# Kernel optimization log

Hardware: AMD Instinct MI355X
Metric: run time of the kernel (lower is better)

## Reference

```python
import jax, jax.numpy as jnp
import numpy as np

N_NODES = 50000
N_EDGES = 800000
IN_C, HID_C, OUT_C = 128, 128, 40


def gcn_conv(x, W, b, src, dst, dinv):
    # x: [N, Fin] -> [N, Fout]; PyG GCNConv: h = W x, then sym-normalized
    # aggregation over edges (incl. self-loops), plus bias.
    h = x @ W  # [N, Fout]
    norm = dinv[src] * dinv[dst]  # [E+N]
    msg = h[src] * norm[:, None]  # gather + scale, [E+N, Fout]
    out = jax.ops.segment_sum(msg, dst, num_segments=x.shape[0])
    return out + b


def _prep_edges(edge_index, n):
    # add self-loops; compute deg^{-1/2} with unit edge weights
    loop = jnp.arange(n, dtype=edge_index.dtype)
    src = jnp.concatenate([edge_index[0], loop])
    dst = jnp.concatenate([edge_index[1], loop])
    deg = jax.ops.segment_sum(jnp.ones_like(dst, dtype=jnp.float32), dst, num_segments=n)
    dinv = jnp.where(deg > 0, jax.lax.rsqrt(jnp.maximum(deg, 1.0)), 0.0)
    return src, dst, dinv


def setup_inputs() -> dict:
    key = jax.random.key(0)
    ks = jax.random.split(key, 5)
    x = jax.random.normal(ks[0], (N_NODES, IN_C), dtype=jnp.float32)
    edge_index = jax.random.randint(ks[1], (2, N_EDGES), 0, N_NODES, dtype=jnp.int32)
    s = 0.05
    W1 = jax.random.normal(ks[2], (IN_C, HID_C), dtype=jnp.float32) * s
    W2 = jax.random.normal(ks[3], (HID_C, HID_C), dtype=jnp.float32) * s
    W3 = jax.random.normal(ks[4], (HID_C, OUT_C), dtype=jnp.float32) * s
    return {
        "x": x, "edge_index": edge_index,
        "W1": W1, "b1": jnp.zeros((HID_C,), jnp.float32),
        "W2": W2, "b2": jnp.zeros((HID_C,), jnp.float32),
        "W3": W3, "b3": jnp.zeros((OUT_C,), jnp.float32),
    }


def reference(x, edge_index, W1, b1, W2, b2, W3, b3):
    n = x.shape[0]
    src, dst, dinv = _prep_edges(edge_index, n)
    h = jax.nn.relu(gcn_conv(x, W1, b1, src, dst, dinv))  # dropout = id (eval)
    h = jax.nn.relu(gcn_conv(h, W2, b2, src, dst, dinv))
    h = gcn_conv(h, W3, b3, src, dst, dinv)
    return jax.nn.log_softmax(h, axis=1)
```

## Files before the change

### kernel.cpp

```cpp
#include <hip/hip_runtime.h>
#include <cmath>

__device__ __forceinline__ unsigned short f2bf(float f) {
  unsigned u = __float_as_uint(f);
  u = (u + 0x7FFFu + ((u >> 16) & 1u)) >> 16;
  return (unsigned short)u;
}
__device__ __forceinline__ unsigned pack2(float a, float b) {
  return (unsigned)f2bf(a) | ((unsigned)f2bf(b) << 16);
}
__device__ __forceinline__ float bflo(unsigned u) { return __uint_as_float(u << 16); }
__device__ __forceinline__ float bfhi(unsigned u) { return __uint_as_float(u & 0xFFFF0000u); }
__device__ __forceinline__ float bf1(unsigned short h) { return __uint_as_float((unsigned)h << 16); }

using bh8 = __attribute__((ext_vector_type(8))) short;
using f32x4 = __attribute__((ext_vector_type(4))) float;

#define BK_STRIDE 8192

__global__ __launch_bounds__(256) void k_f2b(const float* __restrict__ x, unsigned short* __restrict__ xb, int total4) {
  int i = blockIdx.x * 256 + threadIdx.x;
  if (i < total4) {
    float4 v = *(const float4*)&x[(size_t)i * 4];
    uint2 o;
    o.x = pack2(v.x, v.y);
    o.y = pack2(v.z, v.w);
    *(uint2*)&xb[(size_t)i * 4] = o;
  }
}

__global__ __launch_bounds__(256) void k_bin(const int* __restrict__ src, const int* __restrict__ dst,
                                             int* __restrict__ bucketCur, unsigned* __restrict__ bucketBuf,
                                             int E, int chunk) {
  __shared__ int hist[256], base[256], cur[256];
  int t = threadIdx.x;
  hist[t] = 0;
  cur[t] = 0;
  __syncthreads();
  int s0 = blockIdx.x * chunk;
  int s1 = min(E, s0 + chunk);
  for (int i = s0 + t; i < s1; i += 256) atomicAdd(&hist[dst[i] >> 8], 1);
  __syncthreads();
  if (hist[t] > 0) base[t] = atomicAdd(&bucketCur[t], hist[t]);
  __syncthreads();
  for (int i = s0 + t; i < s1; i += 256) {
    int d = dst[i];
    int b = d >> 8;
    int r = base[b] + atomicAdd(&cur[b], 1);
    if (r < BK_STRIDE)
      bucketBuf[(size_t)b * BK_STRIDE + r] = (unsigned)src[i] | ((unsigned)(d & 255) << 16);
  }
}

__global__ __launch_bounds__(256) void k_bucket_scan(const int* __restrict__ bucketCur, int* __restrict__ bucketBase,
                                                     int* __restrict__ rp, int nbk, int n, int E) {
  __shared__ int s[256];
  int t = threadIdx.x;
  int v = (t < nbk) ? bucketCur[t] : 0;
  s[t] = v;
  __syncthreads();
  for (int off = 1; off < 256; off <<= 1) {
    int u = (t >= off) ? s[t - off] : 0;
    __syncthreads();
    s[t] += u;
    __syncthreads();
  }
  if (t < nbk) bucketBase[t] = s[t] - v;
  if (t == 0) rp[n] = E;
}

__global__ __launch_bounds__(256) void k_build(const unsigned* __restrict__ bucketBuf,
                                               const int* __restrict__ bucketCnt,
                                               const int* __restrict__ bucketBase, int* __restrict__ rp,
                                               float* __restrict__ dinv, int* __restrict__ csr, int n) {
  __shared__ int hist[256], excl[256], cur[256], s[256];
  int b = blockIdx.x, t = threadIdx.x;
  int cntE = bucketCnt[b];
  int e0 = bucketBase[b];
  const unsigned* buf = bucketBuf + (size_t)b * BK_STRIDE;
  hist[t] = 0;
  cur[t] = 0;
  __syncthreads();
  for (int i = t; i < cntE; i += 256) atomicAdd(&hist[(buf[i] >> 16) & 255], 1);
  __syncthreads();
  int h = hist[t];
  s[t] = h;
  __syncthreads();
  for (int off = 1; off < 256; off <<= 1) {
    int u = (t >= off) ? s[t - off] : 0;
    __syncthreads();
    s[t] += u;
    __syncthreads();
  }
  excl[t] = s[t] - h;
  int node = (b << 8) + t;
  if (node < n) {
    rp[node] = e0 + excl[t];
    dinv[node] = rsqrtf((float)(h + 1));
  }
  __syncthreads();
  for (int i = t; i < cntE; i += 256) {
    unsigned p = buf[i];
    int lo = (p >> 16) & 255;
    int r = atomicAdd(&cur[lo], 1);
    csr[e0 + excl[lo] + r] = (int)(p & 0xFFFFu);
  }
}

__global__ __launch_bounds__(256) void k_wt_all(const float* __restrict__ W1, const float* __restrict__ W2,
                                                const float* __restrict__ W3, unsigned short* __restrict__ Wt1,
                                                unsigned short* __restrict__ Wt2, unsigned short* __restrict__ Wt3) {
  int i = blockIdx.x * 256 + threadIdx.x;
  if (i < 16384) {
    int c = i >> 7, k = i & 127;
    Wt1[i] = f2bf(W1[(size_t)k * 128 + c]);
  } else if (i < 32768) {
    int j = i - 16384;
    int c = j >> 7, k = j & 127;
    Wt2[j] = f2bf(W2[(size_t)k * 128 + c]);
  } else if (i < 32768 + 6144) {
    int j = i - 32768;
    int c = j >> 7, k = j & 127;
    Wt3[j] = (c < 40) ? f2bf(W3[(size_t)k * 40 + c]) : (unsigned short)0;
  }
}

template <int WT_N, int NW_COL, int MOUT>
__global__ __launch_bounds__(256) void k_mfma_gemm(const unsigned short* __restrict__ A,
                                                   const unsigned short* __restrict__ Bt,
                                                   const float* __restrict__ dinv,
                                                   unsigned short* __restrict__ G, int n) {
  constexpr int NW_ROW = 4 / NW_COL;
  int tid = threadIdx.x;
  int wid = tid >> 6, lane = tid & 63;
  int lr = lane & 15, lq = lane >> 4;
  int wrow = wid / NW_COL, wcol = wid % NW_COL;
  int rowBase = blockIdx.x * (NW_ROW * 32) + wrow * 32;
  int colBase = wcol * (WT_N * 16);

  bh8 af[2][4];
#pragma unroll
  for (int rt = 0; rt < 2; rt++) {
    int row = rowBase + rt * 16 + lr;
    const unsigned short* ap = A + (size_t)row * 128 + lq * 8;
    bool ok = row < n;
#pragma unroll
    for (int ks = 0; ks < 4; ks++) {
      bh8 z = {0, 0, 0, 0, 0, 0, 0, 0};
      af[rt][ks] = ok ? *(const bh8*)(ap + ks * 32) : z;
    }
  }
  bh8 bfr[WT_N][4];
#pragma unroll
  for (int ct = 0; ct < WT_N; ct++) {
    const unsigned short* bp = Bt + (size_t)(colBase + ct * 16 + lr) * 128 + lq * 8;
#pragma unroll
    for (int ks = 0; ks < 4; ks++) bfr[ct][ks] = *(const bh8*)(bp + ks * 32);
  }

  f32x4 acc[2][WT_N];
#pragma unroll
  for (int rt = 0; rt < 2; rt++)
#pragma unroll
    for (int ct = 0; ct < WT_N; ct++) acc[rt][ct] = (f32x4){0.f, 0.f, 0.f, 0.f};

#pragma unroll
  for (int ks = 0; ks < 4; ks++)
#pragma unroll
    for (int rt = 0; rt < 2; rt++)
#pragma unroll
      for (int ct = 0; ct < WT_N; ct++)
        acc[rt][ct] = __builtin_amdgcn_mfma_f32_16x16x32_bf16(af[rt][ks], bfr[ct][ks], acc[rt][ct], 0, 0, 0);

#pragma unroll
  for (int rt = 0; rt < 2; rt++)
#pragma unroll
    for (int r = 0; r < 4; r++) {
      int row = rowBase + rt * 16 + lq * 4 + r;
      if (row < n) {
        float di = dinv[row];
#pragma unroll
        for (int ct = 0; ct < WT_N; ct++) {
          int col = colBase + ct * 16 + lr;
          if (MOUT == 128 || col < MOUT)
            G[(size_t)row * MOUT + col] = f2bf(acc[rt][ct][r] * di);
        }
      }
    }
}

__global__ __launch_bounds__(256) void k_agg_relu128(const unsigned short* __restrict__ g,
                                                     const int* __restrict__ csr, const int* __restrict__ rp,
                                                     const float* __restrict__ dinv, const float* __restrict__ bias,
                                                     unsigned short* __restrict__ out, int n) {
  int t = threadIdx.x;
  int node = blockIdx.x * 8 + (t >> 5);
  if (node >= n) return;
  int c4 = (t & 31) * 4;
  int e0 = rp[node], e1 = rp[node + 1];
  const unsigned short* gp = g + c4;

  float4 a[8];
  {
    uint2 v = *(const uint2*)&gp[(size_t)node * 128];
    a[0] = make_float4(bflo(v.x), bfhi(v.x), bflo(v.y), bfhi(v.y));
  }
#pragma unroll
  for (int u = 1; u < 8; u++) a[u] = make_float4(0.f, 0.f, 0.f, 0.f);

  int e = e0;
  for (; e + 8 <= e1; e += 8) {
    int s[8];
#pragma unroll
    for (int u = 0; u < 8; u++) s[u] = csr[e + u];
#pragma unroll
    for (int u = 0; u < 8; u++) {
      uint2 v = *(const uint2*)&gp[(size_t)s[u] * 128];
      a[u].x += bflo(v.x); a[u].y += bfhi(v.x); a[u].z += bflo(v.y); a[u].w += bfhi(v.y);
    }
  }
  for (; e < e1; ++e) {
    int s = csr[e];
    uint2 v = *(const uint2*)&gp[(size_t)s * 128];
    a[0].x += bflo(v.x); a[0].y += bfhi(v.x); a[0].z += bflo(v.y); a[0].w += bfhi(v.y);
  }
#pragma unroll
  for (int u = 4; u < 8; u++) {
    a[u - 4].x += a[u].x; a[u - 4].y += a[u].y; a[u - 4].z += a[u].z; a[u - 4].w += a[u].w;
  }
#pragma unroll
  for (int u = 2; u < 4; u++) {
    a[u - 2].x += a[u].x; a[u - 2].y += a[u].y; a[u - 2].z += a[u].z; a[u - 2].w += a[u].w;
  }
  float4 acc = make_float4(a[0].x + a[1].x, a[0].y + a[1].y, a[0].z + a[1].z, a[0].w + a[1].w);

  float di = dinv[node];
  float4 bb = *(const float4*)&bias[c4];
  uint2 o;
  o.x = pack2(fmaxf(fmaf(di, acc.x, bb.x), 0.f), fmaxf(fmaf(di, acc.y, bb.y), 0.f));
  o.y = pack2(fmaxf(fmaf(di, acc.z, bb.z), 0.f), fmaxf(fmaf(di, acc.w, bb.w), 0.f));
  *(uint2*)&out[(size_t)node * 128 + c4] = o;
}

__global__ __launch_bounds__(256) void k_agg_lsm40(const unsigned short* __restrict__ g,
                                                   const int* __restrict__ csr, const int* __restrict__ rp,
                                                   const float* __restrict__ dinv, const float* __restrict__ bias,
                                                   float* __restrict__ out, int n) {
  int lane = threadIdx.x & 63;
  int node = blockIdx.x * 4 + (threadIdx.x >> 6);
  if (node >= n) return;
  int e0 = rp[node], e1 = rp[node + 1];

  float a[8];
  a[0] = bf1(g[(size_t)node * 40 + lane]);
#pragma unroll
  for (int u = 1; u < 8; u++) a[u] = 0.f;

  int e = e0;
  for (; e + 8 <= e1; e += 8) {
    int s[8];
#pragma unroll
    for (int u = 0; u < 8; u++) s[u] = csr[e + u];
#pragma unroll
    for (int u = 0; u < 8; u++) a[u] += bf1(g[(size_t)s[u] * 40 + lane]);
  }
  for (; e < e1; ++e) a[0] += bf1(g[(size_t)csr[e] * 40 + lane]);

  float acc = ((a[0] + a[1]) + (a[2] + a[3])) + ((a[4] + a[5]) + (a[6] + a[7]));

  bool act = lane < 40;
  float v = act ? fmaf(dinv[node], acc, bias[lane]) : -INFINITY;
  float m = v;
#pragma unroll
  for (int off = 32; off > 0; off >>= 1) m = fmaxf(m, __shfl_xor(m, off, 64));
  float ex = act ? __expf(v - m) : 0.f;
  float ssum = ex;
#pragma unroll
  for (int off = 32; off > 0; off >>= 1) ssum += __shfl_xor(ssum, off, 64);
  if (act) out[(size_t)node * 40 + lane] = v - m - __logf(ssum);
}


extern "C" void kernel_launch(void* const* d_in, const int* in_sizes, int n_in,
                              void* d_out, int out_size, void* d_ws, size_t ws_size,
                              hipStream_t stream) {
  const float* x  = (const float*)d_in[0];
  const int*   ei = (const int*)d_in[1];
  const float* W1 = (const float*)d_in[2];
  const float* b1 = (const float*)d_in[3];
  const float* W2 = (const float*)d_in[4];
  const float* b2 = (const float*)d_in[5];
  const float* W3 = (const float*)d_in[6];
  const float* b3 = (const float*)d_in[7];
  float* out = (float*)d_out;
  int n = in_sizes[0] / 128;
  int E = in_sizes[1] / 2;
  const int* esrc = ei;
  const int* edst = ei + E;
  int nbk = (n + 255) >> 8;

  size_t off = 0;
  auto alloc = [&](size_t bytes) -> void* {
    void* r = (char*)d_ws + off;
    off += (bytes + 255) & ~(size_t)255;
    return r;
  };
  int*      bucketCur  = (int*)alloc(256 * 4);
  int*      bucketBase = (int*)alloc(257 * 4);
  unsigned* bucketBuf  = (unsigned*)alloc((size_t)nbk * BK_STRIDE * 4);
  int*      rp         = (int*)alloc((size_t)(n + 1) * 4);
  float*    dinv       = (float*)alloc((size_t)n * 4);
  int*      csr        = (int*)alloc((size_t)E * 4);
  unsigned short* xb   = (unsigned short*)alloc((size_t)n * 128 * 2 + 4096);
  unsigned short* bufA = (unsigned short*)alloc((size_t)n * 128 * 2 + 4096);
  unsigned short* bufB = (unsigned short*)alloc((size_t)n * 128 * 2 + 4096);
  unsigned short* Wt1  = (unsigned short*)alloc(128 * 128 * 2);
  unsigned short* Wt2  = (unsigned short*)alloc(128 * 128 * 2);
  unsigned short* Wt3  = (unsigned short*)alloc(48 * 128 * 2);

  hipMemsetAsync(bucketCur, 0, 256 * 4, stream);

  int t4 = n * 128 / 4;
  k_f2b<<<(t4 + 255) / 256, 256, 0, stream>>>(x, xb, t4);

  const int BIN_BLOCKS = 512;
  int chunk = (E + BIN_BLOCKS - 1) / BIN_BLOCKS;
  k_bin<<<BIN_BLOCKS, 256, 0, stream>>>(esrc, edst, bucketCur, bucketBuf, E, chunk);
  k_bucket_scan<<<1, 256, 0, stream>>>(bucketCur, bucketBase, rp, nbk, n, E);
  k_build<<<nbk, 256, 0, stream>>>(bucketBuf, bucketCur, bucketBase, rp, dinv, csr, n);

  k_wt_all<<<(38912 + 255) / 256, 256, 0, stream>>>(W1, W2, W3, Wt1, Wt2, Wt3);

  k_mfma_gemm<4, 2, 128><<<(n + 63) / 64, 256, 0, stream>>>(xb, Wt1, dinv, bufA, n);
  k_agg_relu128<<<(n + 7) / 8, 256, 0, stream>>>(bufA, csr, rp, dinv, b1, bufB, n);
  k_mfma_gemm<4, 2, 128><<<(n + 63) / 64, 256, 0, stream>>>(bufB, Wt2, dinv, bufA, n);
  k_agg_relu128<<<(n + 7) / 8, 256, 0, stream>>>(bufA, csr, rp, dinv, b2, bufB, n);
  k_mfma_gemm<3, 1, 40><<<(n + 127) / 128, 256, 0, stream>>>(bufB, Wt3, dinv, bufA, n);
  k_agg_lsm40<<<(n + 3) / 4, 256, 0, stream>>>(bufA, csr, rp, dinv, b3, out, n);
}
```

Baseline: 206.9 us.

## Store hidden-layer GEMM outputs as custom fp8 and fuse small setup kernels

The first two GEMMs now write their scaled outputs as a custom 8-bit float (4-bit exponent bias-shifted, 3-bit mantissa) instead of bf16. This halves the bytes gathered per edge in the two 128-wide aggregation passes. The bf16 conversion of x is folded into the edge binning kernel, and the weight transpose is merged with the bucket scan, which removes launches. The cost is much lower precision in the intermediate features, which risks accuracy tolerance, plus some extra decode ALU work per gathered element.

```diff
diff --git a/kernel.cpp b/kernel.cpp
--- a/kernel.cpp
+++ b/kernel.cpp
@@ -13,25 +13,27 @@
 __device__ __forceinline__ float bfhi(unsigned u) { return __uint_as_float(u & 0xFFFF0000u); }
 __device__ __forceinline__ float bf1(unsigned short h) { return __uint_as_float((unsigned)h << 16); }
 
+__device__ __forceinline__ unsigned char fp8e(float v) {
+  unsigned u = __float_as_uint(v * 0x1.0p-120f);
+  unsigned s = (u >> 24) & 0x80u;
+  u &= 0x7FFFFFFFu;
+  u = u + 0x000FFFFFu + ((u >> 20) & 1u);
+  return (unsigned char)(s | ((u >> 20) & 0x7Fu));
+}
+__device__ __forceinline__ float fp8d(unsigned b) {
+  unsigned u = ((b & 0x80u) << 24) | ((b & 0x7Fu) << 20);
+  return __uint_as_float(u) * 0x1.0p120f;
+}
+
 using bh8 = __attribute__((ext_vector_type(8))) short;
 using f32x4 = __attribute__((ext_vector_type(4))) float;
 
 #define BK_STRIDE 8192
 
-__global__ __launch_bounds__(256) void k_f2b(const float* __restrict__ x, unsigned short* __restrict__ xb, int total4) {
-  int i = blockIdx.x * 256 + threadIdx.x;
-  if (i < total4) {
-    float4 v = *(const float4*)&x[(size_t)i * 4];
-    uint2 o;
-    o.x = pack2(v.x, v.y);
-    o.y = pack2(v.z, v.w);
-    *(uint2*)&xb[(size_t)i * 4] = o;
-  }
-}
-
 __global__ __launch_bounds__(256) void k_bin(const int* __restrict__ src, const int* __restrict__ dst,
                                              int* __restrict__ bucketCur, unsigned* __restrict__ bucketBuf,
-                                             int E, int chunk) {
+                                             int E, int chunk, const float* __restrict__ x,
+                                             unsigned short* __restrict__ xb, int total4) {
   __shared__ int hist[256], base[256], cur[256];
   int t = threadIdx.x;
   hist[t] = 0;
@@ -50,23 +52,51 @@
     if (r < BK_STRIDE)
       bucketBuf[(size_t)b * BK_STRIDE + r] = (unsigned)src[i] | ((unsigned)(d & 255) << 16);
   }
-}
-
-__global__ __launch_bounds__(256) void k_bucket_scan(const int* __restrict__ bucketCur, int* __restrict__ bucketBase,
-                                                     int* __restrict__ rp, int nbk, int n, int E) {
-  __shared__ int s[256];
+  int tid = blockIdx.x * 256 + t;
+  int stride = gridDim.x * 256;
+  for (int i = tid; i < total4; i += stride) {
+    float4 v = *(const float4*)&x[(size_t)i * 4];
+    uint2 o;
+    o.x = pack2(v.x, v.y);
+    o.y = pack2(v.z, v.w);
+    *(uint2*)&xb[(size_t)i * 4] = o;
+  }
+}
+
+__global__ __launch_bounds__(256) void k_scan_wt(const int* __restrict__ bucketCur, int* __restrict__ bucketBase,
+                                                 int* __restrict__ rp, int nbk, int n, int E,
+                                                 const float* __restrict__ W1, const float* __restrict__ W2,
+                                                 const float* __restrict__ W3, unsigned short* __restrict__ Wt1,
+                                                 unsigned short* __restrict__ Wt2, unsigned short* __restrict__ Wt3) {
   int t = threadIdx.x;
-  int v = (t < nbk) ? bucketCur[t] : 0;
-  s[t] = v;
-  __syncthreads();
-  for (int off = 1; off < 256; off <<= 1) {
-    int u = (t >= off) ? s[t - off] : 0;
+  if (blockIdx.x == 0) {
+    __shared__ int s[256];
+    int v = (t < nbk) ? bucketCur[t] : 0;
+    s[t] = v;
     __syncthreads();
-    s[t] += u;
-    __syncthreads();
-  }
-  if (t < nbk) bucketBase[t] = s[t] - v;
-  if (t == 0) rp[n] = E;
+    for (int off = 1; off < 256; off <<= 1) {
+      int u = (t >= off) ? s[t - off] : 0;
+      __syncthreads();
+      s[t] += u;
+      __syncthreads();
+    }
+    if (t < nbk) bucketBase[t] = s[t] - v;
+    if (t == 0) rp[n] = E;
+    return;
+  }
+  int i = (blockIdx.x - 1) * 256 + t;
+  if (i < 16384) {
+    int c = i >> 7, k = i & 127;
+    Wt1[i] = f2bf(W1[(size_t)k * 128 + c]);
+  } else if (i < 32768) {
+    int j = i - 16384;
+    int c = j >> 7, k = j & 127;
+    Wt2[j] = f2bf(W2[(size_t)k * 128 + c]);
+  } else if (i < 32768 + 6144) {
+    int j = i - 32768;
+    int c = j >> 7, k = j & 127;
+    Wt3[j] = (c < 40) ? f2bf(W3[(size_t)k * 40 + c]) : (unsigned short)0;
+  }
 }
 
 __global__ __launch_bounds__(256) void k_build(const unsigned* __restrict__ bucketBuf,
@@ -107,29 +137,11 @@
   }
 }
 
-__global__ __launch_bounds__(256) void k_wt_all(const float* __restrict__ W1, const float* __restrict__ W2,
-                                                const float* __restrict__ W3, unsigned short* __restrict__ Wt1,
-                                                unsigned short* __restrict__ Wt2, unsigned short* __restrict__ Wt3) {
-  int i = blockIdx.x * 256 + threadIdx.x;
-  if (i < 16384) {
-    int c = i >> 7, k = i & 127;
-    Wt1[i] = f2bf(W1[(size_t)k * 128 + c]);
-  } else if (i < 32768) {
-    int j = i - 16384;
-    int c = j >> 7, k = j & 127;
-    Wt2[j] = f2bf(W2[(size_t)k * 128 + c]);
-  } else if (i < 32768 + 6144) {
-    int j = i - 32768;
-    int c = j >> 7, k = j & 127;
-    Wt3[j] = (c < 40) ? f2bf(W3[(size_t)k * 40 + c]) : (unsigned short)0;
-  }
-}
-
-template <int WT_N, int NW_COL, int MOUT>
+template <int WT_N, int NW_COL, int MOUT, bool OUT8>
 __global__ __launch_bounds__(256) void k_mfma_gemm(const unsigned short* __restrict__ A,
                                                    const unsigned short* __restrict__ Bt,
                                                    const float* __restrict__ dinv,
-                                                   unsigned short* __restrict__ G, int n) {
+                                                   void* __restrict__ Gv, int n) {
   constexpr int NW_ROW = 4 / NW_COL;
   int tid = threadIdx.x;
   int wid = tid >> 6, lane = tid & 63;
@@ -182,28 +194,32 @@
 #pragma unroll
         for (int ct = 0; ct < WT_N; ct++) {
           int col = colBase + ct * 16 + lr;
-          if (MOUT == 128 || col < MOUT)
-            G[(size_t)row * MOUT + col] = f2bf(acc[rt][ct][r] * di);
+          if (MOUT == 128 || col < MOUT) {
+            if constexpr (OUT8)
+              ((unsigned char*)Gv)[(size_t)row * MOUT + col] = fp8e(acc[rt][ct][r] * di);
+            else
+              ((unsigned short*)Gv)[(size_t)row * MOUT + col] = f2bf(acc[rt][ct][r] * di);
+          }
         }
       }
     }
 }
 
-__global__ __launch_bounds__(256) void k_agg_relu128(const unsigned short* __restrict__ g,
-                                                     const int* __restrict__ csr, const int* __restrict__ rp,
-                                                     const float* __restrict__ dinv, const float* __restrict__ bias,
-                                                     unsigned short* __restrict__ out, int n) {
+__global__ __launch_bounds__(256) void k_agg_relu128_f8(const unsigned char* __restrict__ g8,
+                                                        const int* __restrict__ csr, const int* __restrict__ rp,
+                                                        const float* __restrict__ dinv, const float* __restrict__ bias,
+                                                        unsigned short* __restrict__ out, int n) {
   int t = threadIdx.x;
   int node = blockIdx.x * 8 + (t >> 5);
   if (node >= n) return;
-  int c4 = (t & 31) * 4;
+  int c = t & 31;
+  const unsigned* g32 = (const unsigned*)g8;
   int e0 = rp[node], e1 = rp[node + 1];
-  const unsigned short* gp = g + c4;
 
   float4 a[8];
   {
-    uint2 v = *(const uint2*)&gp[(size_t)node * 128];
-    a[0] = make_float4(bflo(v.x), bfhi(v.x), bflo(v.y), bfhi(v.y));
+    unsigned v = g32[(size_t)node * 32 + c];
+    a[0] = make_float4(fp8d(v & 0xFF), fp8d((v >> 8) & 0xFF), fp8d((v >> 16) & 0xFF), fp8d(v >> 24));
   }
 #pragma unroll
   for (int u = 1; u < 8; u++) a[u] = make_float4(0.f, 0.f, 0.f, 0.f);
@@ -213,16 +229,23 @@
     int s[8];
 #pragma unroll
     for (int u = 0; u < 8; u++) s[u] = csr[e + u];
+    unsigned v[8];
+#pragma unroll
+    for (int u = 0; u < 8; u++) v[u] = g32[(size_t)s[u] * 32 + c];
 #pragma unroll
     for (int u = 0; u < 8; u++) {
-      uint2 v = *(const uint2*)&gp[(size_t)s[u] * 128];
-      a[u].x += bflo(v.x); a[u].y += bfhi(v.x); a[u].z += bflo(v.y); a[u].w += bfhi(v.y);
+      a[u].x += fp8d(v[u] & 0xFF);
+      a[u].y += fp8d((v[u] >> 8) & 0xFF);
+      a[u].z += fp8d((v[u] >> 16) & 0xFF);
+      a[u].w += fp8d(v[u] >> 24);
     }
   }
   for (; e < e1; ++e) {
-    int s = csr[e];
-    uint2 v = *(const uint2*)&gp[(size_t)s * 128];
-    a[0].x += bflo(v.x); a[0].y += bfhi(v.x); a[0].z += bflo(v.y); a[0].w += bfhi(v.y);
+    unsigned v = g32[(size_t)csr[e] * 32 + c];
+    a[0].x += fp8d(v & 0xFF);
+    a[0].y += fp8d((v >> 8) & 0xFF);
+    a[0].z += fp8d((v >> 16) & 0xFF);
+    a[0].w += fp8d(v >> 24);
   }
 #pragma unroll
   for (int u = 4; u < 8; u++) {
@@ -235,11 +258,11 @@
   float4 acc = make_float4(a[0].x + a[1].x, a[0].y + a[1].y, a[0].z + a[1].z, a[0].w + a[1].w);
 
   float di = dinv[node];
-  float4 bb = *(const float4*)&bias[c4];
+  float4 bb = *(const float4*)&bias[c * 4];
   uint2 o;
   o.x = pack2(fmaxf(fmaf(di, acc.x, bb.x), 0.f), fmaxf(fmaf(di, acc.y, bb.y), 0.f));
   o.y = pack2(fmaxf(fmaf(di, acc.z, bb.z), 0.f), fmaxf(fmaf(di, acc.w, bb.w), 0.f));
-  *(uint2*)&out[(size_t)node * 128 + c4] = o;
+  *(uint2*)&out[(size_t)node * 128 + c * 4] = o;
 }
 
 __global__ __launch_bounds__(256) void k_agg_lsm40(const unsigned short* __restrict__ g,
@@ -312,29 +335,26 @@
   float*    dinv       = (float*)alloc((size_t)n * 4);
   int*      csr        = (int*)alloc((size_t)E * 4);
   unsigned short* xb   = (unsigned short*)alloc((size_t)n * 128 * 2 + 4096);
-  unsigned short* bufA = (unsigned short*)alloc((size_t)n * 128 * 2 + 4096);
   unsigned short* bufB = (unsigned short*)alloc((size_t)n * 128 * 2 + 4096);
+  unsigned char*  gq   = (unsigned char*)alloc((size_t)n * 128 + 4096);
   unsigned short* Wt1  = (unsigned short*)alloc(128 * 128 * 2);
   unsigned short* Wt2  = (unsigned short*)alloc(128 * 128 * 2);
   unsigned short* Wt3  = (unsigned short*)alloc(48 * 128 * 2);
 
   hipMemsetAsync(bucketCur, 0, 256 * 4, stream);
 
-  int t4 = n * 128 / 4;
-  k_f2b<<<(t4 + 255) / 256, 256, 0, stream>>>(x, xb, t4);
-
   const int BIN_BLOCKS = 512;
   int chunk = (E + BIN_BLOCKS - 1) / BIN_BLOCKS;
-  k_bin<<<BIN_BLOCKS, 256, 0, stream>>>(esrc, edst, bucketCur, bucketBuf, E, chunk);
-  k_bucket_scan<<<1, 256, 0, stream>>>(bucketCur, bucketBase, rp, nbk, n, E);
+  int t4 = n * 128 / 4;
+  k_bin<<<BIN_BLOCKS, 256, 0, stream>>>(esrc, edst, bucketCur, bucketBuf, E, chunk, x, xb, t4);
+  k_scan_wt<<<1 + 152, 256, 0, stream>>>(bucketCur, bucketBase, rp, nbk, n, E, W1, W2, W3, Wt1, Wt2, Wt3);
   k_build<<<nbk, 256, 0, stream>>>(bucketBuf, bucketCur, bucketBase, rp, dinv, csr, n);
 
-  k_wt_all<<<(38912 + 255) / 256, 256, 0, stream>>>(W1, W2, W3, Wt1, Wt2, Wt3);
-
-  k_mfma_gemm<4, 2, 128><<<(n + 63) / 64, 256, 0, stream>>>(xb, Wt1, dinv, bufA, n);
-  k_agg_relu128<<<(n + 7) / 8, 256, 0, stream>>>(bufA, csr, rp, dinv, b1, bufB, n);
-  k_mfma_gemm<4, 2, 128><<<(n + 63) / 64, 256, 0, stream>>>(bufB, Wt2, dinv, bufA, n);
-  k_agg_relu128<<<(n + 7) / 8, 256, 0, stream>>>(bufA, csr, rp, dinv, b2, bufB, n);
-  k_mfma_gemm<3, 1, 40><<<(n + 127) / 128, 256, 0, stream>>>(bufB, Wt3, dinv, bufA, n);
-  k_agg_lsm40<<<(n + 3) / 4, 256, 0, stream>>>(bufA, csr, rp, dinv, b3, out, n);
-}
+  k_mfma_gemm<4, 2, 128, true><<<(n + 63) / 64, 256, 0, stream>>>(xb, Wt1, dinv, gq, n);
+  k_agg_relu128_f8<<<(n + 7) / 8, 256, 0, stream>>>(gq, csr, rp, dinv, b1, bufB, n);
+  k_mfma_gemm<4, 2, 128, true><<<(n + 63) / 64, 256, 0, stream>>>(bufB, Wt2, dinv, gq, n);
+  k_agg_relu128_f8<<<(n + 7) / 8, 256, 0, stream>>>(gq, csr, rp, dinv, b2, xb, n);
+  unsigned short* g3 = (unsigned short*)gq;
+  k_mfma_gemm<3, 1, 40, false><<<(n + 127) / 128, 256, 0, stream>>>(xb, Wt3, dinv, g3, n);
+  k_agg_lsm40<<<(n + 3) / 4, 256, 0, stream>>>(g3, csr, rp, dinv, b3, out, n);
+}
```

Measured after the change: 202.1 us. 1.02x faster.
